# Kernel optimization log

Hardware: AMD Instinct MI355X
Metric: run time of the kernel (lower is better)

The kernel has to match this reference:

```python
import jax, jax.numpy as jnp
import numpy as np
import math

L, Bt, IN, H = 512, 128, 512, 60


def setup_inputs() -> dict:
    key = jax.random.key(0)
    k1, k2, k3 = jax.random.split(key, 3)
    inp = jax.random.normal(k1, (L, Bt, IN), dtype=jnp.float32)
    W = jax.random.normal(k2, (H, IN), dtype=jnp.float32) / np.sqrt(IN)
    b = jnp.zeros((H,), dtype=jnp.float32)
    alphabet = jax.random.uniform(k3, (H, 3), dtype=jnp.float32, minval=-math.pi, maxval=math.pi)
    bond_lengths = jnp.array([132.868, 145.801, 152.326], dtype=jnp.float32)
    bond_angles = jnp.array([2.028, 2.124, 1.941], dtype=jnp.float32)
    return {"inp": inp, "W": W, "b": b, "alphabet": alphabet,
            "bond_lengths": bond_lengths, "bond_angles": bond_angles}


def reference(inp, W, b, alphabet, bond_lengths, bond_angles):
    Lr, Bb = inp.shape[0], inp.shape[1]
    # mixture over alphabet of torsion angles
    x = jax.nn.softmax(inp @ W.T + b, axis=2)                 # (L, B, H)
    phi = jnp.arctan2(x @ jnp.sin(alphabet), x @ jnp.cos(alphabet))  # (L, B, 3)
    # per residue i the loop consumes phi[i].T -> bond index is fastest axis
    phi_f = phi.transpose(0, 2, 1).reshape(Lr * 3, Bb)        # (3L, B)
    r = jnp.tile(bond_lengths, Lr)[:, None]                   # (3L, 1)
    th = jnp.tile(bond_angles, Lr)[:, None]                   # (3L, 1)
    # SRF coordinates of every new atom
    c_tilde = jnp.stack([
        (r * jnp.cos(th)) * jnp.ones_like(phi_f),
        r * jnp.cos(phi_f) * jnp.sin(th),
        r * jnp.sin(phi_f) * jnp.sin(th),
    ], axis=-1)                                               # (3L, B, 3)

    e = jnp.eye(3, dtype=inp.dtype)
    carry0 = (jnp.broadcast_to(e[0], (Bb, 3)),
              jnp.broadcast_to(e[1], (Bb, 3)),
              jnp.broadcast_to(e[2], (Bb, 3)))

    def step(carry, ct):
        A, Bp, C = carry                                      # each (B, 3)
        BC = C - Bp
        bc = BC / jnp.linalg.norm(BC, axis=1, keepdims=True)
        AB = Bp - A
        Nv = jnp.cross(AB, bc)
        n = Nv / jnp.linalg.norm(Nv, axis=1, keepdims=True)
        # D = C + R @ c_tilde, R columns = [bc, n x bc, n]
        D = C + bc * ct[:, 0:1] + jnp.cross(n, bc) * ct[:, 1:2] + n * ct[:, 2:3]
        return (Bp, C, D), D

    _, coords = jax.lax.scan(step, carry0, c_tilde)           # (3L, B, 3)
    return coords
```

## Files before the change

kernel.cpp:

```cpp
#include <hip/hip_runtime.h>
#include <math.h>

#define LSEQ  512
#define BT    128
#define INF   512
#define HH    60
#define NSTEP 1536
#define CHUNK 24

#define MTILE 128
#define KTILE 64
#define APAD  72

typedef __attribute__((ext_vector_type(8))) short bf16x8;
typedef __attribute__((ext_vector_type(4))) float floatx4;

__device__ __forceinline__ unsigned short bf16_rn(float x) {
  unsigned u = __float_as_uint(x);
  return (unsigned short)((u + 0x7FFFu + ((u >> 16) & 1u)) >> 16);
}
__device__ __forceinline__ void split2(float x, unsigned short& h, unsigned short& l) {
  h = bf16_rn(x);
  float hf = __uint_as_float(((unsigned)h) << 16);
  l = bf16_rn(x - hf);
}

__global__ __launch_bounds__(256) void k_wconv(
    const float* __restrict__ W, unsigned short* __restrict__ Wh,
    unsigned short* __restrict__ Wl) {
  const int idx = blockIdx.x * 256 + threadIdx.x;
  const int h = idx >> 9, k = idx & 511;
  float x = (h < HH) ? W[h * INF + k] : 0.f;
  unsigned short hb, lb; split2(x, hb, lb);
  Wh[idx] = hb; Wl[idx] = lb;
}

__global__ __launch_bounds__(256, 2) void k_phi(
    const float* __restrict__ inp, const unsigned short* __restrict__ Wh,
    const unsigned short* __restrict__ Wl, const float* __restrict__ bias,
    const float* __restrict__ alphabet, float* __restrict__ phi_out) {
  __shared__ unsigned short Ah[MTILE * APAD];
  __shared__ unsigned short Al[MTILE * APAD];
  __shared__ float sS[HH * 3], sC[HH * 3], sBias[64];

  const int tid  = threadIdx.x;
  const int lane = tid & 63;
  const int wid  = tid >> 6;
  const int c    = lane & 15;
  const int quad = lane >> 4;
  const int row0 = blockIdx.x * MTILE;

  if (tid < HH * 3) { float a = alphabet[tid]; sS[tid] = __sinf(a); sC[tid] = __cosf(a); }
  if (tid >= 192 && tid < 256) { int n = tid - 192; sBias[n] = (n < HH) ? bias[n] : 0.f; }

  floatx4 acc[2][4];
#pragma unroll
  for (int mt = 0; mt < 2; ++mt)
#pragma unroll
    for (int nt = 0; nt < 4; ++nt) acc[mt][nt] = (floatx4){0.f, 0.f, 0.f, 0.f};

  for (int t = 0; t < INF / KTILE; ++t) {
    const int k0 = t * KTILE;
#pragma unroll
    for (int i = 0; i < 8; ++i) {
      const int f4i = i * 256 + tid;
      const int r   = f4i >> 4;
      const int c4  = f4i & 15;
      float4 v = *(const float4*)(inp + (size_t)(row0 + r) * INF + k0 + 4 * c4);
      unsigned short h0,l0,h1,l1,h2,l2,h3,l3;
      split2(v.x, h0, l0); split2(v.y, h1, l1);
      split2(v.z, h2, l2); split2(v.w, h3, l3);
      uint2 ph = make_uint2((unsigned)h0 | ((unsigned)h1 << 16),
                            (unsigned)h2 | ((unsigned)h3 << 16));
      uint2 pl = make_uint2((unsigned)l0 | ((unsigned)l1 << 16),
                            (unsigned)l2 | ((unsigned)l3 << 16));
      *(uint2*)&Ah[r * APAD + 4 * c4] = ph;
      *(uint2*)&Al[r * APAD + 4 * c4] = pl;
    }
    __syncthreads();

#pragma unroll
    for (int ks = 0; ks < 2; ++ks) {
      const int kl = ks * 32;
      const int kg = k0 + kl;
      bf16x8 Bh[4], Bl[4];
#pragma unroll
      for (int nt = 0; nt < 4; ++nt) {
        const int h = nt * 16 + c;
        Bh[nt] = *(const bf16x8*)(Wh + (size_t)h * INF + kg + quad * 8);
        Bl[nt] = *(const bf16x8*)(Wl + (size_t)h * INF + kg + quad * 8);
      }
      bf16x8 Af[2], Alf[2];
#pragma unroll
      for (int mt = 0; mt < 2; ++mt) {
        const int m = wid * 32 + mt * 16 + c;
        Af[mt]  = *(const bf16x8*)(&Ah[m * APAD + kl + quad * 8]);
        Alf[mt] = *(const bf16x8*)(&Al[m * APAD + kl + quad * 8]);
      }
#pragma unroll
      for (int mt = 0; mt < 2; ++mt)
#pragma unroll
        for (int nt = 0; nt < 4; ++nt) {
          acc[mt][nt] = __builtin_amdgcn_mfma_f32_16x16x32_bf16(Af[mt],  Bh[nt], acc[mt][nt], 0, 0, 0);
          acc[mt][nt] = __builtin_amdgcn_mfma_f32_16x16x32_bf16(Af[mt],  Bl[nt], acc[mt][nt], 0, 0, 0);
          acc[mt][nt] = __builtin_amdgcn_mfma_f32_16x16x32_bf16(Alf[mt], Bh[nt], acc[mt][nt], 0, 0, 0);
        }
    }
    __syncthreads();
  }

#pragma unroll
  for (int mt = 0; mt < 2; ++mt) {
#pragma unroll
    for (int reg = 0; reg < 4; ++reg) {
      float lg[4];  bool val[4];
#pragma unroll
      for (int nt = 0; nt < 4; ++nt) {
        const int n = nt * 16 + c;
        val[nt] = (n < HH);
        lg[nt] = acc[mt][nt][reg] + sBias[n];
      }
      float m = -1e30f;
#pragma unroll
      for (int nt = 0; nt < 4; ++nt) if (val[nt]) m = fmaxf(m, lg[nt]);
#pragma unroll
      for (int d = 1; d < 16; d <<= 1) m = fmaxf(m, __shfl_xor(m, d, 64));

      float s0=0.f,c0=0.f,s1=0.f,c1=0.f,s2=0.f,c2=0.f;
#pragma unroll
      for (int nt = 0; nt < 4; ++nt) {
        const int n = nt * 16 + c;
        float e = val[nt] ? __expf(lg[nt] - m) : 0.f;
        s0 = fmaf(e, sS[n*3+0], s0);  c0 = fmaf(e, sC[n*3+0], c0);
        s1 = fmaf(e, sS[n*3+1], s1);  c1 = fmaf(e, sC[n*3+1], c1);
        s2 = fmaf(e, sS[n*3+2], s2);  c2 = fmaf(e, sC[n*3+2], c2);
      }
#pragma unroll
      for (int d = 1; d < 16; d <<= 1) {
        s0 += __shfl_xor(s0, d, 64);  c0 += __shfl_xor(c0, d, 64);
        s1 += __shfl_xor(s1, d, 64);  c1 += __shfl_xor(c1, d, 64);
        s2 += __shfl_xor(s2, d, 64);  c2 += __shfl_xor(c2, d, 64);
      }
      if (c == 0) {
        const int row = row0 + wid * 32 + mt * 16 + quad * 4 + reg;
        const int l  = row >> 7;
        const int bb = row & 127;
        float* pp = phi_out + (size_t)bb * NSTEP + 3 * l;
        pp[0] = atan2f(s0, c0);
        pp[1] = atan2f(s1, c1);
        pp[2] = atan2f(s2, c2);
      }
    }
  }
}

struct Xf { float r[9]; float p[3]; };

__device__ __forceinline__ Xf compose(const Xf& A, const Xf& B) {
  Xf o;
#pragma unroll
  for (int i = 0; i < 3; ++i) {
#pragma unroll
    for (int j = 0; j < 3; ++j) {
      o.r[i*3+j] = fmaf(A.r[i*3+0], B.r[0+j],
                   fmaf(A.r[i*3+1], B.r[3+j],
                        A.r[i*3+2] * B.r[6+j]));
    }
    o.p[i] = fmaf(A.r[i*3+0], B.p[0],
             fmaf(A.r[i*3+1], B.p[1],
             fmaf(A.r[i*3+2], B.p[2], A.p[i])));
  }
  return o;
}

__device__ __forceinline__ Xf make_T(float phi, float st, float ct, float r) {
  float sp = __sinf(phi), cp = __cosf(phi);
  Xf T;
  T.r[0] = ct;      T.r[1] = -st;     T.r[2] = 0.f;
  T.r[3] = cp * st; T.r[4] = ct * cp; T.r[5] = -sp;
  T.r[6] = sp * st; T.r[7] = ct * sp; T.r[8] = cp;
  T.p[0] = r * ct;  T.p[1] = r * T.r[3]; T.p[2] = r * T.r[6];
  return T;
}

__device__ __forceinline__ void set_identity(Xf& X) {
  X.r[0]=1.f; X.r[1]=0.f; X.r[2]=0.f;
  X.r[3]=0.f; X.r[4]=1.f; X.r[5]=0.f;
  X.r[6]=0.f; X.r[7]=0.f; X.r[8]=1.f;
  X.p[0]=0.f; X.p[1]=0.f; X.p[2]=0.f;
}

__global__ __launch_bounds__(64) void k_scan(
    const float* __restrict__ phi, const float* __restrict__ bl,
    const float* __restrict__ ba, float* __restrict__ out) {
  const int b = blockIdx.x;
  const int t = threadIdx.x;

  float st[3], ct[3], rr[3];
#pragma unroll
  for (int j = 0; j < 3; ++j) {
    float a = ba[j];
    st[j] = __sinf(a); ct[j] = __cosf(a); rr[j] = bl[j];
  }

  float f[CHUNK];
  const float4* ph4 = (const float4*)(phi + (size_t)b * NSTEP + t * CHUNK);
#pragma unroll
  for (int q = 0; q < CHUNK/4; ++q) {
    float4 v = ph4[q];
    f[4*q+0] = v.x; f[4*q+1] = v.y; f[4*q+2] = v.z; f[4*q+3] = v.w;
  }

  Xf Q = make_T(f[0], st[0], ct[0], rr[0]);
#pragma unroll
  for (int s = 1; s < CHUNK; ++s)
    Q = compose(Q, make_T(f[s], st[s%3], ct[s%3], rr[s%3]));

#pragma unroll
  for (int d = 1; d < 64; d <<= 1) {
    Xf O;
#pragma unroll
    for (int q = 0; q < 9; ++q) O.r[q] = __shfl_up(Q.r[q], d, 64);
#pragma unroll
    for (int q = 0; q < 3; ++q) O.p[q] = __shfl_up(Q.p[q], d, 64);
    if (t < d) set_identity(O);
    Q = compose(O, Q);
  }

  Xf E;
#pragma unroll
  for (int q = 0; q < 9; ++q) E.r[q] = __shfl_up(Q.r[q], 1, 64);
#pragma unroll
  for (int q = 0; q < 3; ++q) E.p[q] = __shfl_up(Q.p[q], 1, 64);
  if (t == 0) set_identity(E);

  Xf S0;
  S0.r[0] = 0.f;                  S0.r[1] = 0.816496580927726f;   S0.r[2] = 0.5773502691896258f;
  S0.r[3] = -0.7071067811865475f; S0.r[4] = -0.4082482904638631f; S0.r[5] = 0.5773502691896258f;
  S0.r[6] = 0.7071067811865475f;  S0.r[7] = -0.4082482904638631f; S0.r[8] = 0.5773502691896258f;
  S0.p[0] = 0.f; S0.p[1] = 0.f; S0.p[2] = 1.f;

  Xf cur = compose(S0, E);

  float* op = out + (size_t)(t * CHUNK) * (BT * 3) + b * 3;
#pragma unroll
  for (int s = 0; s < CHUNK; ++s) {
    cur = compose(cur, make_T(f[s], st[s%3], ct[s%3], rr[s%3]));
    op[(size_t)s * (BT*3) + 0] = cur.p[0];
    op[(size_t)s * (BT*3) + 1] = cur.p[1];
    op[(size_t)s * (BT*3) + 2] = cur.p[2];
  }
}

extern "C" void kernel_launch(void* const* d_in, const int* in_sizes, int n_in,
                              void* d_out, int out_size, void* d_ws, size_t ws_size,
                              hipStream_t stream) {
  const float* inp      = (const float*)d_in[0];
  const float* W        = (const float*)d_in[1];
  const float* bias     = (const float*)d_in[2];
  const float* alphabet = (const float*)d_in[3];
  const float* bl       = (const float*)d_in[4];
  const float* ba       = (const float*)d_in[5];
  float* out = (float*)d_out;

  float* phi = (float*)d_ws;
  unsigned short* Wh = (unsigned short*)((char*)d_ws + 786432);
  unsigned short* Wl = Wh + 64 * INF;

  k_wconv<<<dim3(128), dim3(256), 0, stream>>>(W, Wh, Wl);
  k_phi<<<dim3((LSEQ*BT)/MTILE), dim3(256), 0, stream>>>(inp, Wh, Wl, bias, alphabet, phi);
  k_scan<<<dim3(BT), dim3(64), 0, stream>>>(phi, bl, ba, out);
}
```

Measured before the change: 232.0 us.

## Load GEMM A fragments directly from global into registers, drop LDS staging

The phi GEMM kernel no longer stages the fp32 input tile through shared memory as split bf16 hi/lo halves. Each lane now loads its own 8 contiguous floats per row fragment straight from global memory, splits them in registers, and feeds the MFMA. This removes the LDS writes and reads and the two barriers per K tile, and frees LDS for occupancy. In exchange the per-lane global loads are 32-byte strided rows, which may coalesce less well, and the compute-heavy scan kernel probably dominates runtime anyway.

```diff
diff --git a/kernel.cpp b/kernel.cpp
--- a/kernel.cpp
+++ b/kernel.cpp
@@ -9,8 +9,6 @@
 #define CHUNK 24
 
 #define MTILE 128
-#define KTILE 64
-#define APAD  72
 
 typedef __attribute__((ext_vector_type(8))) short bf16x8;
 typedef __attribute__((ext_vector_type(4))) float floatx4;
@@ -39,8 +37,6 @@
     const float* __restrict__ inp, const unsigned short* __restrict__ Wh,
     const unsigned short* __restrict__ Wl, const float* __restrict__ bias,
     const float* __restrict__ alphabet, float* __restrict__ phi_out) {
-  __shared__ unsigned short Ah[MTILE * APAD];
-  __shared__ unsigned short Al[MTILE * APAD];
   __shared__ float sS[HH * 3], sC[HH * 3], sBias[64];
 
   const int tid  = threadIdx.x;
@@ -59,55 +55,47 @@
 #pragma unroll
     for (int nt = 0; nt < 4; ++nt) acc[mt][nt] = (floatx4){0.f, 0.f, 0.f, 0.f};
 
-  for (int t = 0; t < INF / KTILE; ++t) {
-    const int k0 = t * KTILE;
-#pragma unroll
-    for (int i = 0; i < 8; ++i) {
-      const int f4i = i * 256 + tid;
-      const int r   = f4i >> 4;
-      const int c4  = f4i & 15;
-      float4 v = *(const float4*)(inp + (size_t)(row0 + r) * INF + k0 + 4 * c4);
-      unsigned short h0,l0,h1,l1,h2,l2,h3,l3;
-      split2(v.x, h0, l0); split2(v.y, h1, l1);
-      split2(v.z, h2, l2); split2(v.w, h3, l3);
-      uint2 ph = make_uint2((unsigned)h0 | ((unsigned)h1 << 16),
-                            (unsigned)h2 | ((unsigned)h3 << 16));
-      uint2 pl = make_uint2((unsigned)l0 | ((unsigned)l1 << 16),
-                            (unsigned)l2 | ((unsigned)l3 << 16));
-      *(uint2*)&Ah[r * APAD + 4 * c4] = ph;
-      *(uint2*)&Al[r * APAD + 4 * c4] = pl;
-    }
-    __syncthreads();
-
-#pragma unroll
-    for (int ks = 0; ks < 2; ++ks) {
-      const int kl = ks * 32;
-      const int kg = k0 + kl;
-      bf16x8 Bh[4], Bl[4];
+  const float* a0p = inp + (size_t)(row0 + wid * 32 + c)      * INF + quad * 8;
+  const float* a1p = inp + (size_t)(row0 + wid * 32 + 16 + c) * INF + quad * 8;
+  const unsigned short* whp = Wh + (size_t)c * INF + quad * 8;
+  const unsigned short* wlp = Wl + (size_t)c * INF + quad * 8;
+
+#pragma unroll 2
+  for (int ks = 0; ks < INF / 32; ++ks) {
+    const int kg = ks * 32;
+    float4 a00 = *(const float4*)(a0p + kg);
+    float4 a01 = *(const float4*)(a0p + kg + 4);
+    float4 a10 = *(const float4*)(a1p + kg);
+    float4 a11 = *(const float4*)(a1p + kg + 4);
+    bf16x8 Bh[4], Bl[4];
+#pragma unroll
+    for (int nt = 0; nt < 4; ++nt) {
+      Bh[nt] = *(const bf16x8*)(whp + (size_t)(nt * 16) * INF + kg);
+      Bl[nt] = *(const bf16x8*)(wlp + (size_t)(nt * 16) * INF + kg);
+    }
+    bf16x8 Ah[2], Al[2];
+    {
+      float av[2][8] = {{a00.x,a00.y,a00.z,a00.w,a01.x,a01.y,a01.z,a01.w},
+                        {a10.x,a10.y,a10.z,a10.w,a11.x,a11.y,a11.z,a11.w}};
+#pragma unroll
+      for (int mt = 0; mt < 2; ++mt)
+#pragma unroll
+        for (int j = 0; j < 8; ++j) {
+          unsigned short hb, lb; split2(av[mt][j], hb, lb);
+          Ah[mt][j] = (short)hb; Al[mt][j] = (short)lb;
+        }
+    }
+#pragma unroll
+    for (int mt = 0; mt < 2; ++mt)
 #pragma unroll
       for (int nt = 0; nt < 4; ++nt) {
-        const int h = nt * 16 + c;
-        Bh[nt] = *(const bf16x8*)(Wh + (size_t)h * INF + kg + quad * 8);
-        Bl[nt] = *(const bf16x8*)(Wl + (size_t)h * INF + kg + quad * 8);
-      }
-      bf16x8 Af[2], Alf[2];
-#pragma unroll
-      for (int mt = 0; mt < 2; ++mt) {
-        const int m = wid * 32 + mt * 16 + c;
-        Af[mt]  = *(const bf16x8*)(&Ah[m * APAD + kl + quad * 8]);
-        Alf[mt] = *(const bf16x8*)(&Al[m * APAD + kl + quad * 8]);
-      }
-#pragma unroll
-      for (int mt = 0; mt < 2; ++mt)
-#pragma unroll
-        for (int nt = 0; nt < 4; ++nt) {
-          acc[mt][nt] = __builtin_amdgcn_mfma_f32_16x16x32_bf16(Af[mt],  Bh[nt], acc[mt][nt], 0, 0, 0);
-          acc[mt][nt] = __builtin_amdgcn_mfma_f32_16x16x32_bf16(Af[mt],  Bl[nt], acc[mt][nt], 0, 0, 0);
-          acc[mt][nt] = __builtin_amdgcn_mfma_f32_16x16x32_bf16(Alf[mt], Bh[nt], acc[mt][nt], 0, 0, 0);
-        }
-    }
-    __syncthreads();
-  }
+        acc[mt][nt] = __builtin_amdgcn_mfma_f32_16x16x32_bf16(Ah[mt], Bh[nt], acc[mt][nt], 0, 0, 0);
+        acc[mt][nt] = __builtin_amdgcn_mfma_f32_16x16x32_bf16(Ah[mt], Bl[nt], acc[mt][nt], 0, 0, 0);
+        acc[mt][nt] = __builtin_amdgcn_mfma_f32_16x16x32_bf16(Al[mt], Bh[nt], acc[mt][nt], 0, 0, 0);
+      }
+  }
+
+  __syncthreads();
 
 #pragma unroll
   for (int mt = 0; mt < 2; ++mt) {
```

Measured after the change: 234.0 us. About the same (+0.9%).
